# Kernel optimization log

Hardware: AMD Instinct MI355X
Metric: run time of the kernel (lower is better)

Reference implementation:

```python
import jax, jax.numpy as jnp
import numpy as np

EOS = 1e-10
N = 6000          # nnodes
E = 192000        # n_edges (avg degree 32)
D_IN = 512        # input_dim
H = 128           # hidden_dim
ALPHA = 1.0
TEMP = 1.0
BIAS = 1e-4


def setup_inputs() -> dict:
    key = jax.random.key(0)
    k1, k2, k3, k4, k5, k6, k7 = jax.random.split(key, 7)
    features = jax.random.normal(k1, (N, D_IN), dtype=jnp.float32)
    edges = jax.random.randint(k2, (2, E), 0, N)
    # params: embedding Linear(D_IN->H) and edge MLP Linear(2H->1)
    w_emb = jax.random.normal(k3, (D_IN, H), dtype=jnp.float32) * 0.05
    b_emb = jnp.zeros((H,), jnp.float32)
    w_mlp = jax.random.normal(k4, (2 * H, 1), dtype=jnp.float32) * 0.05
    b_mlp = jnp.zeros((1,), jnp.float32)
    # gumbel-sigmoid noise: eps = (bias-(1-bias))*u + (1-bias)  in [bias, 1-bias]
    u = jax.random.uniform(k5, (E,), dtype=jnp.float32)
    eps = (BIAS - (1.0 - BIAS)) * u + (1.0 - BIAS)
    gate_noise = jnp.log(eps) - jnp.log(1.0 - eps)
    return {"features": features, "edges": edges, "w_emb": w_emb, "b_emb": b_emb,
            "w_mlp": w_mlp, "b_mlp": b_mlp, "gate_noise": gate_noise}


def _normalize_sym(adj):
    d = adj.sum(axis=1)
    inv = 1.0 / (jnp.sqrt(d) + EOS)
    return adj * inv[:, None] * inv[None, :]


def reference(features, edges, w_emb, b_emb, w_mlp, b_mlp, gate_noise):
    # node embeddings: single Linear + ReLU
    emb = jax.nn.relu(features @ w_emb + b_emb)              # [N, H]
    h0 = emb[edges[0]]                                       # [E, H]
    h1 = emb[edges[1]]                                       # [E, H]
    s1 = (jnp.concatenate([h0, h1], axis=1) @ w_mlp + b_mlp).ravel()
    s2 = (jnp.concatenate([h1, h0], axis=1) @ w_mlp + b_mlp).ravel()
    raw = (s1 + s2) * 0.5                                    # [E]
    # gumbel-sigmoid gating
    weights_lp = jax.nn.sigmoid((gate_noise + raw) / TEMP)
    weights_hp = 1.0 - weights_lp

    eye = jnp.eye(N, dtype=features.dtype)

    def build_adj(w):
        adj = jnp.zeros((N, N), features.dtype).at[edges[0], edges[1]].set(w)
        return _normalize_sym(adj + eye)

    adj_lp = build_adj(weights_lp)
    adj_hp = build_adj(weights_hp)
    mask = jnp.zeros((N, N), features.dtype).at[edges[0], edges[1]].set(1.0)
    adj_hp = eye - adj_hp * mask * ALPHA
    adj_unnorm = jnp.zeros((N, N), features.dtype).at[edges[0], edges[1]].set(1.0)
    return (adj_lp, adj_hp, weights_lp, weights_hp, adj_unnorm)
```

## Files before the change

### kernel.cpp

```cpp
#include <hip/hip_runtime.h>
#include <math.h>

#define NNODES 6000
#define NEDGES 192000
#define DIN 512
#define HDIM 128
#define ALPHA 1.0f
#define EOS 1e-10f

static const size_t NN = (size_t)NNODES * (size_t)NNODES;

typedef float vfloat4 __attribute__((ext_vector_type(4)));

__global__ __launch_bounds__(256) void zero3_kernel(
    vfloat4* __restrict__ a, size_t na, vfloat4* __restrict__ b, size_t nb,
    vfloat4* __restrict__ c, size_t nc) {
  const size_t stride = (size_t)gridDim.x * blockDim.x;
  const size_t i = (size_t)blockIdx.x * blockDim.x + threadIdx.x;
  const vfloat4 z = {0.f, 0.f, 0.f, 0.f};
  for (size_t k = i; k < na; k += stride) __builtin_nontemporal_store(z, a + k);
  for (size_t k = i; k < nb; k += stride) __builtin_nontemporal_store(z, b + k);
  for (size_t k = i; k < nc; k += stride) c[k] = z;
}

__global__ __launch_bounds__(64) void embed_g_kernel(
    const float* __restrict__ feat, const float* __restrict__ w_emb,
    const float* __restrict__ b_emb, const float* __restrict__ w_mlp,
    const float* __restrict__ b_mlp, float* __restrict__ g) {
  __shared__ float sf[4 * DIN];
  const int t = threadIdx.x;
  const int nb = blockIdx.x * 4;

  const float4* f4 = (const float4*)(feat + (size_t)nb * DIN);
  float4* s4 = (float4*)sf;
#pragma unroll
  for (int k = 0; k < 8; ++k) s4[k * 64 + t] = f4[k * 64 + t];
  __syncthreads();

  const int h0 = t, h1 = t + 64;
  float acc0[4], acc1[4];
  const float b0 = b_emb[h0], b1 = b_emb[h1];
#pragma unroll
  for (int n = 0; n < 4; ++n) { acc0[n] = b0; acc1[n] = b1; }

  for (int d = 0; d < DIN; d += 4) {
    float w00 = w_emb[(d + 0) * HDIM + h0];
    float w01 = w_emb[(d + 1) * HDIM + h0];
    float w02 = w_emb[(d + 2) * HDIM + h0];
    float w03 = w_emb[(d + 3) * HDIM + h0];
    float w10 = w_emb[(d + 0) * HDIM + h1];
    float w11 = w_emb[(d + 1) * HDIM + h1];
    float w12 = w_emb[(d + 2) * HDIM + h1];
    float w13 = w_emb[(d + 3) * HDIM + h1];
#pragma unroll
    for (int n = 0; n < 4; ++n) {
      const float4 f = *(const float4*)&sf[n * DIN + d];
      acc0[n] += f.x * w00;
      acc0[n] += f.y * w01;
      acc0[n] += f.z * w02;
      acc0[n] += f.w * w03;
      acc1[n] += f.x * w10;
      acc1[n] += f.y * w11;
      acc1[n] += f.z * w12;
      acc1[n] += f.w * w13;
    }
  }

  const float wv0 = 0.5f * (w_mlp[h0] + w_mlp[HDIM + h0]);
  const float wv1 = 0.5f * (w_mlp[h1] + w_mlp[HDIM + h1]);
  const float half_b = 0.5f * b_mlp[0];
#pragma unroll
  for (int n = 0; n < 4; ++n) {
    float v = fmaxf(acc0[n], 0.0f) * wv0 + fmaxf(acc1[n], 0.0f) * wv1;
#pragma unroll
    for (int off = 32; off > 0; off >>= 1) v += __shfl_down(v, off, 64);
    if (t == 0) g[nb + n] = v + half_b;
  }
}

__global__ __launch_bounds__(256) void edge_weights_kernel(
    const int* __restrict__ edges, const float* __restrict__ g,
    const float* __restrict__ noise, float* __restrict__ w_lp,
    float* __restrict__ w_hp, int* __restrict__ winner) {
  const int e = blockIdx.x * blockDim.x + threadIdx.x;
  if (e >= NEDGES) return;
  const int u = edges[e];
  const int v = edges[NEDGES + e];
  const float x = noise[e] + g[u] + g[v];
  const float wl = 1.0f / (1.0f + expf(-x));
  const float wh = 1.0f - wl;
  w_lp[e] = wl;
  w_hp[e] = wh;
  atomicMax(&winner[(size_t)u * NNODES + v], e + 1);
}

__global__ __launch_bounds__(256) void edge_deg_kernel(
    const int* __restrict__ edges, const float* __restrict__ w_lp,
    const float* __restrict__ w_hp, const int* __restrict__ winner,
    float* __restrict__ deg_lp, float* __restrict__ deg_hp) {
  const int e = blockIdx.x * blockDim.x + threadIdx.x;
  if (e >= NEDGES) return;
  const int u = edges[e];
  const int v = edges[NEDGES + e];
  if (winner[(size_t)u * NNODES + v] != e + 1) return;
  atomicAdd(&deg_lp[u], w_lp[e]);
  atomicAdd(&deg_hp[u], w_hp[e]);
}

__global__ __launch_bounds__(256) void node_inv_kernel(
    const float* __restrict__ deg_lp, const float* __restrict__ deg_hp,
    float* __restrict__ inv_lp, float* __restrict__ inv_hp,
    float* __restrict__ adj_lp, float* __restrict__ adj_hp) {
  const int i = blockIdx.x * blockDim.x + threadIdx.x;
  if (i >= NNODES) return;
  const float il = 1.0f / (sqrtf(deg_lp[i] + 1.0f) + EOS);
  const float ih = 1.0f / (sqrtf(deg_hp[i] + 1.0f) + EOS);
  inv_lp[i] = il;
  inv_hp[i] = ih;
  const size_t diag = (size_t)i * NNODES + i;
  adj_lp[diag] = il * il;
  adj_hp[diag] = 1.0f;
}

__global__ __launch_bounds__(256) void edge_write_kernel(
    const int* __restrict__ edges, const float* __restrict__ w_lp,
    const float* __restrict__ w_hp, const float* __restrict__ inv_lp,
    const float* __restrict__ inv_hp, float* __restrict__ adj_lp,
    float* __restrict__ adj_hp, float* __restrict__ unnorm) {
  const int e = blockIdx.x * blockDim.x + threadIdx.x;
  if (e >= NEDGES) return;
  const int u = edges[e];
  const int v = edges[NEDGES + e];
  const size_t cell = (size_t)u * NNODES + v;
  const int win = ((const int*)unnorm)[cell];
  if (win != e + 1) return;
  const float wl = w_lp[e];
  const float wh = w_hp[e];
  const float il = inv_lp[u] * inv_lp[v];
  const float ih = inv_hp[u] * inv_hp[v];
  if (u == v) {
    adj_lp[cell] = (wl + 1.0f) * il;
    adj_hp[cell] = 1.0f - (wh + 1.0f) * ih * ALPHA;
  } else {
    adj_lp[cell] = wl * il;
    adj_hp[cell] = -wh * ih * ALPHA;
  }
  unnorm[cell] = 1.0f;
}

extern "C" void kernel_launch(void* const* d_in, const int* in_sizes, int n_in,
                              void* d_out, int out_size, void* d_ws,
                              size_t ws_size, hipStream_t stream) {
  const float* feat  = (const float*)d_in[0];
  const int*   edges = (const int*)d_in[1];
  const float* w_emb = (const float*)d_in[2];
  const float* b_emb = (const float*)d_in[3];
  const float* w_mlp = (const float*)d_in[4];
  const float* b_mlp = (const float*)d_in[5];
  const float* noise = (const float*)d_in[6];

  float* out    = (float*)d_out;
  float* adj_lp = out;
  float* adj_hp = out + NN;
  float* w_lp   = out + 2 * NN;
  float* w_hp   = w_lp + NEDGES;
  float* unnorm = w_hp + NEDGES;

  float* deg_lp = (float*)d_ws;
  float* deg_hp = deg_lp + NNODES;
  float* inv_lp = deg_hp + NNODES;
  float* inv_hp = inv_lp + NNODES;
  float* g      = inv_hp + NNODES;

  zero3_kernel<<<4096, 256, 0, stream>>>(
      (vfloat4*)adj_lp, (2 * NN) / 4, (vfloat4*)unnorm, NN / 4,
      (vfloat4*)deg_lp, (2 * NNODES) / 4);

  embed_g_kernel<<<NNODES / 4, 64, 0, stream>>>(feat, w_emb, b_emb, w_mlp,
                                                b_mlp, g);

  const int eb = (NEDGES + 255) / 256;
  edge_weights_kernel<<<eb, 256, 0, stream>>>(edges, g, noise, w_lp, w_hp,
                                              (int*)unnorm);
  edge_deg_kernel<<<eb, 256, 0, stream>>>(edges, w_lp, w_hp,
                                          (const int*)unnorm, deg_lp, deg_hp);
  node_inv_kernel<<<(NNODES + 255) / 256, 256, 0, stream>>>(
      deg_lp, deg_hp, inv_lp, inv_hp, adj_lp, adj_hp);
  edge_write_kernel<<<eb, 256, 0, stream>>>(edges, w_lp, w_hp, inv_lp, inv_hp,
                                            adj_lp, adj_hp, unnorm);
}
```

Before: 618.8 us.

## Fuse all stages into one cooperative kernel with grid-wide syncs

Replaces the six separate launches (zero, embed, edge weights, degree, inverse-sqrt, edge write) with a single cooperative kernel that uses grid.sync between phases. The embedding loop now processes 16 nodes per 256-thread block via a grid-stride loop. The aim is to remove per-launch overhead and inter-kernel gaps. In exchange it costs grid-wide barriers and a capped grid size that may lower memory-fill parallelism.

```diff
diff --git a/kernel.cpp b/kernel.cpp
--- a/kernel.cpp
+++ b/kernel.cpp
@@ -1,151 +1,154 @@
 #include <hip/hip_runtime.h>
+#include <hip/hip_cooperative_groups.h>
 #include <math.h>
+
+namespace cg = cooperative_groups;
 
 #define NNODES 6000
 #define NEDGES 192000
 #define DIN 512
 #define HDIM 128
-#define ALPHA 1.0f
 #define EOS 1e-10f
 
 static const size_t NN = (size_t)NNODES * (size_t)NNODES;
 
 typedef float vfloat4 __attribute__((ext_vector_type(4)));
 
-__global__ __launch_bounds__(256) void zero3_kernel(
-    vfloat4* __restrict__ a, size_t na, vfloat4* __restrict__ b, size_t nb,
-    vfloat4* __restrict__ c, size_t nc) {
-  const size_t stride = (size_t)gridDim.x * blockDim.x;
-  const size_t i = (size_t)blockIdx.x * blockDim.x + threadIdx.x;
-  const vfloat4 z = {0.f, 0.f, 0.f, 0.f};
-  for (size_t k = i; k < na; k += stride) __builtin_nontemporal_store(z, a + k);
-  for (size_t k = i; k < nb; k += stride) __builtin_nontemporal_store(z, b + k);
-  for (size_t k = i; k < nc; k += stride) c[k] = z;
-}
+__global__ __launch_bounds__(256, 3) void fused_kernel(
+    const float* __restrict__ feat, const int* __restrict__ edges,
+    const float* __restrict__ w_emb, const float* __restrict__ b_emb,
+    const float* __restrict__ w_mlp, const float* __restrict__ b_mlp,
+    const float* __restrict__ noise, float* __restrict__ adj_lp,
+    float* __restrict__ adj_hp, float* __restrict__ w_lp,
+    float* __restrict__ w_hp, float* __restrict__ unnorm,
+    float* __restrict__ deg_lp, float* __restrict__ deg_hp,
+    float* __restrict__ inv_lp, float* __restrict__ inv_hp,
+    float* __restrict__ g) {
+  cg::grid_group grid = cg::this_grid();
+  const int tid = threadIdx.x;
+  const size_t gtid = (size_t)blockIdx.x * blockDim.x + tid;
+  const size_t gstride = (size_t)gridDim.x * blockDim.x;
 
-__global__ __launch_bounds__(64) void embed_g_kernel(
-    const float* __restrict__ feat, const float* __restrict__ w_emb,
-    const float* __restrict__ b_emb, const float* __restrict__ w_mlp,
-    const float* __restrict__ b_mlp, float* __restrict__ g) {
-  __shared__ float sf[4 * DIN];
-  const int t = threadIdx.x;
-  const int nb = blockIdx.x * 4;
+  __shared__ float sf[16 * DIN];
 
-  const float4* f4 = (const float4*)(feat + (size_t)nb * DIN);
-  float4* s4 = (float4*)sf;
+  {
+    const vfloat4 z = {0.f, 0.f, 0.f, 0.f};
+    vfloat4* a = (vfloat4*)adj_lp;
+    for (size_t k = gtid; k < (2 * NN) / 4; k += gstride)
+      __builtin_nontemporal_store(z, a + k);
+    vfloat4* b = (vfloat4*)unnorm;
+    for (size_t k = gtid; k < NN / 4; k += gstride)
+      __builtin_nontemporal_store(z, b + k);
+    vfloat4* c = (vfloat4*)deg_lp;
+    for (size_t k = gtid; k < (2 * NNODES) / 4; k += gstride) c[k] = z;
+  }
+
+  for (int bg = blockIdx.x; bg < NNODES / 16; bg += gridDim.x) {
+    const float4* f4 = (const float4*)(feat + (size_t)bg * 16 * DIN);
+    float4* s4 = (float4*)sf;
 #pragma unroll
-  for (int k = 0; k < 8; ++k) s4[k * 64 + t] = f4[k * 64 + t];
-  __syncthreads();
+    for (int k = 0; k < 8; ++k) s4[k * 256 + tid] = f4[k * 256 + tid];
+    __syncthreads();
 
-  const int h0 = t, h1 = t + 64;
-  float acc0[4], acc1[4];
-  const float b0 = b_emb[h0], b1 = b_emb[h1];
+    const int wave = tid >> 6, lane = tid & 63;
+    const float* sw = sf + wave * (4 * DIN);
+    const int h0 = lane, h1 = lane + 64;
+    float acc0[4], acc1[4];
+    const float bb0 = b_emb[h0], bb1 = b_emb[h1];
 #pragma unroll
-  for (int n = 0; n < 4; ++n) { acc0[n] = b0; acc1[n] = b1; }
+    for (int n = 0; n < 4; ++n) { acc0[n] = bb0; acc1[n] = bb1; }
 
-  for (int d = 0; d < DIN; d += 4) {
-    float w00 = w_emb[(d + 0) * HDIM + h0];
-    float w01 = w_emb[(d + 1) * HDIM + h0];
-    float w02 = w_emb[(d + 2) * HDIM + h0];
-    float w03 = w_emb[(d + 3) * HDIM + h0];
-    float w10 = w_emb[(d + 0) * HDIM + h1];
-    float w11 = w_emb[(d + 1) * HDIM + h1];
-    float w12 = w_emb[(d + 2) * HDIM + h1];
-    float w13 = w_emb[(d + 3) * HDIM + h1];
+    for (int d = 0; d < DIN; d += 4) {
+      const float w00 = w_emb[(d + 0) * HDIM + h0];
+      const float w01 = w_emb[(d + 1) * HDIM + h0];
+      const float w02 = w_emb[(d + 2) * HDIM + h0];
+      const float w03 = w_emb[(d + 3) * HDIM + h0];
+      const float w10 = w_emb[(d + 0) * HDIM + h1];
+      const float w11 = w_emb[(d + 1) * HDIM + h1];
+      const float w12 = w_emb[(d + 2) * HDIM + h1];
+      const float w13 = w_emb[(d + 3) * HDIM + h1];
+#pragma unroll
+      for (int n = 0; n < 4; ++n) {
+        const float4 f = *(const float4*)&sw[n * DIN + d];
+        acc0[n] += f.x * w00;
+        acc0[n] += f.y * w01;
+        acc0[n] += f.z * w02;
+        acc0[n] += f.w * w03;
+        acc1[n] += f.x * w10;
+        acc1[n] += f.y * w11;
+        acc1[n] += f.z * w12;
+        acc1[n] += f.w * w13;
+      }
+    }
+
+    const float wv0 = 0.5f * (w_mlp[h0] + w_mlp[HDIM + h0]);
+    const float wv1 = 0.5f * (w_mlp[h1] + w_mlp[HDIM + h1]);
+    const float half_b = 0.5f * b_mlp[0];
+    const int node0 = bg * 16 + wave * 4;
 #pragma unroll
     for (int n = 0; n < 4; ++n) {
-      const float4 f = *(const float4*)&sf[n * DIN + d];
-      acc0[n] += f.x * w00;
-      acc0[n] += f.y * w01;
-      acc0[n] += f.z * w02;
-      acc0[n] += f.w * w03;
-      acc1[n] += f.x * w10;
-      acc1[n] += f.y * w11;
-      acc1[n] += f.z * w12;
-      acc1[n] += f.w * w13;
+      float v = fmaxf(acc0[n], 0.0f) * wv0 + fmaxf(acc1[n], 0.0f) * wv1;
+#pragma unroll
+      for (int off = 32; off > 0; off >>= 1) v += __shfl_down(v, off, 64);
+      if (lane == 0) g[node0 + n] = v + half_b;
     }
+    __syncthreads();
   }
 
-  const float wv0 = 0.5f * (w_mlp[h0] + w_mlp[HDIM + h0]);
-  const float wv1 = 0.5f * (w_mlp[h1] + w_mlp[HDIM + h1]);
-  const float half_b = 0.5f * b_mlp[0];
-#pragma unroll
-  for (int n = 0; n < 4; ++n) {
-    float v = fmaxf(acc0[n], 0.0f) * wv0 + fmaxf(acc1[n], 0.0f) * wv1;
-#pragma unroll
-    for (int off = 32; off > 0; off >>= 1) v += __shfl_down(v, off, 64);
-    if (t == 0) g[nb + n] = v + half_b;
+  grid.sync();
+
+  for (size_t e = gtid; e < NEDGES; e += gstride) {
+    const int u = edges[e];
+    const int v = edges[NEDGES + e];
+    const float x = noise[e] + g[u] + g[v];
+    const float wl = 1.0f / (1.0f + expf(-x));
+    w_lp[e] = wl;
+    w_hp[e] = 1.0f - wl;
+    atomicMax((int*)unnorm + ((size_t)u * NNODES + v), (int)e + 1);
   }
-}
 
-__global__ __launch_bounds__(256) void edge_weights_kernel(
-    const int* __restrict__ edges, const float* __restrict__ g,
-    const float* __restrict__ noise, float* __restrict__ w_lp,
-    float* __restrict__ w_hp, int* __restrict__ winner) {
-  const int e = blockIdx.x * blockDim.x + threadIdx.x;
-  if (e >= NEDGES) return;
-  const int u = edges[e];
-  const int v = edges[NEDGES + e];
-  const float x = noise[e] + g[u] + g[v];
-  const float wl = 1.0f / (1.0f + expf(-x));
-  const float wh = 1.0f - wl;
-  w_lp[e] = wl;
-  w_hp[e] = wh;
-  atomicMax(&winner[(size_t)u * NNODES + v], e + 1);
-}
+  grid.sync();
 
-__global__ __launch_bounds__(256) void edge_deg_kernel(
-    const int* __restrict__ edges, const float* __restrict__ w_lp,
-    const float* __restrict__ w_hp, const int* __restrict__ winner,
-    float* __restrict__ deg_lp, float* __restrict__ deg_hp) {
-  const int e = blockIdx.x * blockDim.x + threadIdx.x;
-  if (e >= NEDGES) return;
-  const int u = edges[e];
-  const int v = edges[NEDGES + e];
-  if (winner[(size_t)u * NNODES + v] != e + 1) return;
-  atomicAdd(&deg_lp[u], w_lp[e]);
-  atomicAdd(&deg_hp[u], w_hp[e]);
-}
+  for (size_t e = gtid; e < NEDGES; e += gstride) {
+    const int u = edges[e];
+    const int v = edges[NEDGES + e];
+    if (((const int*)unnorm)[(size_t)u * NNODES + v] != (int)e + 1) continue;
+    atomicAdd(&deg_lp[u], w_lp[e]);
+    atomicAdd(&deg_hp[u], w_hp[e]);
+  }
 
-__global__ __launch_bounds__(256) void node_inv_kernel(
-    const float* __restrict__ deg_lp, const float* __restrict__ deg_hp,
-    float* __restrict__ inv_lp, float* __restrict__ inv_hp,
-    float* __restrict__ adj_lp, float* __restrict__ adj_hp) {
-  const int i = blockIdx.x * blockDim.x + threadIdx.x;
-  if (i >= NNODES) return;
-  const float il = 1.0f / (sqrtf(deg_lp[i] + 1.0f) + EOS);
-  const float ih = 1.0f / (sqrtf(deg_hp[i] + 1.0f) + EOS);
-  inv_lp[i] = il;
-  inv_hp[i] = ih;
-  const size_t diag = (size_t)i * NNODES + i;
-  adj_lp[diag] = il * il;
-  adj_hp[diag] = 1.0f;
-}
+  grid.sync();
 
-__global__ __launch_bounds__(256) void edge_write_kernel(
-    const int* __restrict__ edges, const float* __restrict__ w_lp,
-    const float* __restrict__ w_hp, const float* __restrict__ inv_lp,
-    const float* __restrict__ inv_hp, float* __restrict__ adj_lp,
-    float* __restrict__ adj_hp, float* __restrict__ unnorm) {
-  const int e = blockIdx.x * blockDim.x + threadIdx.x;
-  if (e >= NEDGES) return;
-  const int u = edges[e];
-  const int v = edges[NEDGES + e];
-  const size_t cell = (size_t)u * NNODES + v;
-  const int win = ((const int*)unnorm)[cell];
-  if (win != e + 1) return;
-  const float wl = w_lp[e];
-  const float wh = w_hp[e];
-  const float il = inv_lp[u] * inv_lp[v];
-  const float ih = inv_hp[u] * inv_hp[v];
-  if (u == v) {
-    adj_lp[cell] = (wl + 1.0f) * il;
-    adj_hp[cell] = 1.0f - (wh + 1.0f) * ih * ALPHA;
-  } else {
-    adj_lp[cell] = wl * il;
-    adj_hp[cell] = -wh * ih * ALPHA;
+  for (size_t i = gtid; i < NNODES; i += gstride) {
+    const float il = 1.0f / (sqrtf(deg_lp[i] + 1.0f) + EOS);
+    const float ih = 1.0f / (sqrtf(deg_hp[i] + 1.0f) + EOS);
+    inv_lp[i] = il;
+    inv_hp[i] = ih;
+    const size_t dg = (size_t)i * NNODES + i;
+    adj_lp[dg] = il * il;
+    adj_hp[dg] = 1.0f;
   }
-  unnorm[cell] = 1.0f;
+
+  grid.sync();
+
+  for (size_t e = gtid; e < NEDGES; e += gstride) {
+    const int u = edges[e];
+    const int v = edges[NEDGES + e];
+    const size_t cell = (size_t)u * NNODES + v;
+    if (((const int*)unnorm)[cell] != (int)e + 1) continue;
+    const float wl = w_lp[e];
+    const float wh = w_hp[e];
+    const float il = inv_lp[u] * inv_lp[v];
+    const float ih = inv_hp[u] * inv_hp[v];
+    if (u == v) {
+      adj_lp[cell] = (wl + 1.0f) * il;
+      adj_hp[cell] = 1.0f - (wh + 1.0f) * ih;
+    } else {
+      adj_lp[cell] = wl * il;
+      adj_hp[cell] = -wh * ih;
+    }
+    unnorm[cell] = 1.0f;
+  }
 }
 
 extern "C" void kernel_launch(void* const* d_in, const int* in_sizes, int n_in,
@@ -172,20 +175,17 @@
   float* inv_hp = inv_lp + NNODES;
   float* g      = inv_hp + NNODES;
 
-  zero3_kernel<<<4096, 256, 0, stream>>>(
-      (vfloat4*)adj_lp, (2 * NN) / 4, (vfloat4*)unnorm, NN / 4,
-      (vfloat4*)deg_lp, (2 * NNODES) / 4);
+  int bpc = 0;
+  hipOccupancyMaxActiveBlocksPerMultiprocessor(&bpc, fused_kernel, 256, 0);
+  int nblk = bpc * 256;
+  if (nblk > 768) nblk = 768;
 
-  embed_g_kernel<<<NNODES / 4, 64, 0, stream>>>(feat, w_emb, b_emb, w_mlp,
-                                                b_mlp, g);
-
-  const int eb = (NEDGES + 255) / 256;
-  edge_weights_kernel<<<eb, 256, 0, stream>>>(edges, g, noise, w_lp, w_hp,
-                                              (int*)unnorm);
-  edge_deg_kernel<<<eb, 256, 0, stream>>>(edges, w_lp, w_hp,
-                                          (const int*)unnorm, deg_lp, deg_hp);
-  node_inv_kernel<<<(NNODES + 255) / 256, 256, 0, stream>>>(
-      deg_lp, deg_hp, inv_lp, inv_hp, adj_lp, adj_hp);
-  edge_write_kernel<<<eb, 256, 0, stream>>>(edges, w_lp, w_hp, inv_lp, inv_hp,
-                                            adj_lp, adj_hp, unnorm);
+  void* kargs[] = {(void*)&feat,   (void*)&edges,  (void*)&w_emb,
+                   (void*)&b_emb,  (void*)&w_mlp,  (void*)&b_mlp,
+                   (void*)&noise,  (void*)&adj_lp, (void*)&adj_hp,
+                   (void*)&w_lp,   (void*)&w_hp,   (void*)&unnorm,
+                   (void*)&deg_lp, (void*)&deg_hp, (void*)&inv_lp,
+                   (void*)&inv_hp, (void*)&g};
+  hipLaunchCooperativeKernel(fused_kernel, dim3(nblk), dim3(256), kargs, 0,
+                             stream);
 }
```

After: 812.9 us. 1.31x slower.

## Track duplicate-edge winners in a hash table instead of the dense matrix

Applied to the files above, without the earlier changes.

Edge deduplication now uses an open-addressing hash table in workspace (CAS on keys, atomicMax on values) rather than atomics on the dense unnorm matrix. This keeps scattered atomics and lookups in a small, cache-friendly region instead of a huge output buffer. The embedding kernel processes 8 nodes per block, and the zero kernel uses plain stores with a larger grid. It adds linear probing cost and zeroing of the table, and drops nontemporal stores.

```diff
diff --git a/kernel.cpp b/kernel.cpp
--- a/kernel.cpp
+++ b/kernel.cpp
@@ -5,21 +5,26 @@
 #define NEDGES 192000
 #define DIN 512
 #define HDIM 128
-#define ALPHA 1.0f
 #define EOS 1e-10f
 
+#define HSLOTS (1 << 20)
+#define HMASK (HSLOTS - 1)
+
 static const size_t NN = (size_t)NNODES * (size_t)NNODES;
 
-typedef float vfloat4 __attribute__((ext_vector_type(4)));
-
-__global__ __launch_bounds__(256) void zero3_kernel(
-    vfloat4* __restrict__ a, size_t na, vfloat4* __restrict__ b, size_t nb,
-    vfloat4* __restrict__ c, size_t nc) {
+__device__ __forceinline__ unsigned hash_cell(unsigned cell) {
+  return (cell * 2654435761u >> 11) & HMASK;
+}
+
+__global__ __launch_bounds__(256) void zero_kernel(
+    float4* __restrict__ a, size_t na,
+    float4* __restrict__ b, size_t nb,
+    float4* __restrict__ c, size_t nc) {
   const size_t stride = (size_t)gridDim.x * blockDim.x;
   const size_t i = (size_t)blockIdx.x * blockDim.x + threadIdx.x;
-  const vfloat4 z = {0.f, 0.f, 0.f, 0.f};
-  for (size_t k = i; k < na; k += stride) __builtin_nontemporal_store(z, a + k);
-  for (size_t k = i; k < nb; k += stride) __builtin_nontemporal_store(z, b + k);
+  const float4 z = make_float4(0.f, 0.f, 0.f, 0.f);
+  for (size_t k = i; k < na; k += stride) a[k] = z;
+  for (size_t k = i; k < nb; k += stride) b[k] = z;
   for (size_t k = i; k < nc; k += stride) c[k] = z;
 }
 
@@ -27,33 +32,33 @@
     const float* __restrict__ feat, const float* __restrict__ w_emb,
     const float* __restrict__ b_emb, const float* __restrict__ w_mlp,
     const float* __restrict__ b_mlp, float* __restrict__ g) {
-  __shared__ float sf[4 * DIN];
+  __shared__ float sf[8 * DIN];
   const int t = threadIdx.x;
-  const int nb = blockIdx.x * 4;
+  const int nb = blockIdx.x * 8;
 
   const float4* f4 = (const float4*)(feat + (size_t)nb * DIN);
   float4* s4 = (float4*)sf;
 #pragma unroll
-  for (int k = 0; k < 8; ++k) s4[k * 64 + t] = f4[k * 64 + t];
+  for (int k = 0; k < 16; ++k) s4[k * 64 + t] = f4[k * 64 + t];
   __syncthreads();
 
   const int h0 = t, h1 = t + 64;
-  float acc0[4], acc1[4];
+  float acc0[8], acc1[8];
   const float b0 = b_emb[h0], b1 = b_emb[h1];
 #pragma unroll
-  for (int n = 0; n < 4; ++n) { acc0[n] = b0; acc1[n] = b1; }
+  for (int n = 0; n < 8; ++n) { acc0[n] = b0; acc1[n] = b1; }
 
   for (int d = 0; d < DIN; d += 4) {
-    float w00 = w_emb[(d + 0) * HDIM + h0];
-    float w01 = w_emb[(d + 1) * HDIM + h0];
-    float w02 = w_emb[(d + 2) * HDIM + h0];
-    float w03 = w_emb[(d + 3) * HDIM + h0];
-    float w10 = w_emb[(d + 0) * HDIM + h1];
-    float w11 = w_emb[(d + 1) * HDIM + h1];
-    float w12 = w_emb[(d + 2) * HDIM + h1];
-    float w13 = w_emb[(d + 3) * HDIM + h1];
-#pragma unroll
-    for (int n = 0; n < 4; ++n) {
+    const float w00 = w_emb[(d + 0) * HDIM + h0];
+    const float w01 = w_emb[(d + 1) * HDIM + h0];
+    const float w02 = w_emb[(d + 2) * HDIM + h0];
+    const float w03 = w_emb[(d + 3) * HDIM + h0];
+    const float w10 = w_emb[(d + 0) * HDIM + h1];
+    const float w11 = w_emb[(d + 1) * HDIM + h1];
+    const float w12 = w_emb[(d + 2) * HDIM + h1];
+    const float w13 = w_emb[(d + 3) * HDIM + h1];
+#pragma unroll
+    for (int n = 0; n < 8; ++n) {
       const float4 f = *(const float4*)&sf[n * DIN + d];
       acc0[n] += f.x * w00;
       acc0[n] += f.y * w01;
@@ -70,7 +75,7 @@
   const float wv1 = 0.5f * (w_mlp[h1] + w_mlp[HDIM + h1]);
   const float half_b = 0.5f * b_mlp[0];
 #pragma unroll
-  for (int n = 0; n < 4; ++n) {
+  for (int n = 0; n < 8; ++n) {
     float v = fmaxf(acc0[n], 0.0f) * wv0 + fmaxf(acc1[n], 0.0f) * wv1;
 #pragma unroll
     for (int off = 32; off > 0; off >>= 1) v += __shfl_down(v, off, 64);
@@ -81,28 +86,45 @@
 __global__ __launch_bounds__(256) void edge_weights_kernel(
     const int* __restrict__ edges, const float* __restrict__ g,
     const float* __restrict__ noise, float* __restrict__ w_lp,
-    float* __restrict__ w_hp, int* __restrict__ winner) {
+    float* __restrict__ w_hp, int* __restrict__ hkeys,
+    int* __restrict__ hvals) {
   const int e = blockIdx.x * blockDim.x + threadIdx.x;
-  if (e >= NEDGES) return;
   const int u = edges[e];
   const int v = edges[NEDGES + e];
   const float x = noise[e] + g[u] + g[v];
   const float wl = 1.0f / (1.0f + expf(-x));
-  const float wh = 1.0f - wl;
   w_lp[e] = wl;
-  w_hp[e] = wh;
-  atomicMax(&winner[(size_t)u * NNODES + v], e + 1);
+  w_hp[e] = 1.0f - wl;
+
+  const unsigned cell = (unsigned)u * NNODES + (unsigned)v;
+  unsigned idx = hash_cell(cell);
+  const int key = (int)cell + 1;
+  while (true) {
+    const int k = atomicCAS(&hkeys[idx], 0, key);
+    if (k == 0 || k == key) { atomicMax(&hvals[idx], e + 1); break; }
+    idx = (idx + 1) & HMASK;
+  }
+}
+
+__device__ __forceinline__ int hash_winner(const int* __restrict__ hkeys,
+                                           const int* __restrict__ hvals,
+                                           unsigned cell) {
+  unsigned idx = hash_cell(cell);
+  const int key = (int)cell + 1;
+  while (hkeys[idx] != key) idx = (idx + 1) & HMASK;
+  return hvals[idx];
 }
 
 __global__ __launch_bounds__(256) void edge_deg_kernel(
     const int* __restrict__ edges, const float* __restrict__ w_lp,
-    const float* __restrict__ w_hp, const int* __restrict__ winner,
-    float* __restrict__ deg_lp, float* __restrict__ deg_hp) {
+    const float* __restrict__ w_hp, const int* __restrict__ hkeys,
+    const int* __restrict__ hvals, float* __restrict__ deg_lp,
+    float* __restrict__ deg_hp) {
   const int e = blockIdx.x * blockDim.x + threadIdx.x;
-  if (e >= NEDGES) return;
   const int u = edges[e];
   const int v = edges[NEDGES + e];
-  if (winner[(size_t)u * NNODES + v] != e + 1) return;
+  if (hash_winner(hkeys, hvals, (unsigned)u * NNODES + (unsigned)v) != e + 1)
+    return;
   atomicAdd(&deg_lp[u], w_lp[e]);
   atomicAdd(&deg_hp[u], w_hp[e]);
 }
@@ -117,33 +139,33 @@
   const float ih = 1.0f / (sqrtf(deg_hp[i] + 1.0f) + EOS);
   inv_lp[i] = il;
   inv_hp[i] = ih;
-  const size_t diag = (size_t)i * NNODES + i;
-  adj_lp[diag] = il * il;
-  adj_hp[diag] = 1.0f;
+  const size_t dg = (size_t)i * NNODES + i;
+  adj_lp[dg] = il * il;
+  adj_hp[dg] = 1.0f;
 }
 
 __global__ __launch_bounds__(256) void edge_write_kernel(
     const int* __restrict__ edges, const float* __restrict__ w_lp,
     const float* __restrict__ w_hp, const float* __restrict__ inv_lp,
-    const float* __restrict__ inv_hp, float* __restrict__ adj_lp,
+    const float* __restrict__ inv_hp, const int* __restrict__ hkeys,
+    const int* __restrict__ hvals, float* __restrict__ adj_lp,
     float* __restrict__ adj_hp, float* __restrict__ unnorm) {
   const int e = blockIdx.x * blockDim.x + threadIdx.x;
-  if (e >= NEDGES) return;
   const int u = edges[e];
   const int v = edges[NEDGES + e];
+  const unsigned cell32 = (unsigned)u * NNODES + (unsigned)v;
+  if (hash_winner(hkeys, hvals, cell32) != e + 1) return;
   const size_t cell = (size_t)u * NNODES + v;
-  const int win = ((const int*)unnorm)[cell];
-  if (win != e + 1) return;
   const float wl = w_lp[e];
   const float wh = w_hp[e];
   const float il = inv_lp[u] * inv_lp[v];
   const float ih = inv_hp[u] * inv_hp[v];
   if (u == v) {
     adj_lp[cell] = (wl + 1.0f) * il;
-    adj_hp[cell] = 1.0f - (wh + 1.0f) * ih * ALPHA;
+    adj_hp[cell] = 1.0f - (wh + 1.0f) * ih;
   } else {
     adj_lp[cell] = wl * il;
-    adj_hp[cell] = -wh * ih * ALPHA;
+    adj_hp[cell] = -wh * ih;
   }
   unnorm[cell] = 1.0f;
 }
@@ -166,26 +188,30 @@
   float* w_hp   = w_lp + NEDGES;
   float* unnorm = w_hp + NEDGES;
 
-  float* deg_lp = (float*)d_ws;
+  int*   hkeys  = (int*)d_ws;
+  int*   hvals  = hkeys + HSLOTS;
+  float* deg_lp = (float*)(hvals + HSLOTS);
   float* deg_hp = deg_lp + NNODES;
   float* inv_lp = deg_hp + NNODES;
   float* inv_hp = inv_lp + NNODES;
   float* g      = inv_hp + NNODES;
 
-  zero3_kernel<<<4096, 256, 0, stream>>>(
-      (vfloat4*)adj_lp, (2 * NN) / 4, (vfloat4*)unnorm, NN / 4,
-      (vfloat4*)deg_lp, (2 * NNODES) / 4);
-
-  embed_g_kernel<<<NNODES / 4, 64, 0, stream>>>(feat, w_emb, b_emb, w_mlp,
+  const size_t nc = (2 * (size_t)HSLOTS + 2 * NNODES) / 4;
+  zero_kernel<<<8192, 256, 0, stream>>>((float4*)adj_lp, (2 * NN) / 4,
+                                        (float4*)unnorm, NN / 4,
+                                        (float4*)hkeys, nc);
+
+  embed_g_kernel<<<NNODES / 8, 64, 0, stream>>>(feat, w_emb, b_emb, w_mlp,
                                                 b_mlp, g);
 
-  const int eb = (NEDGES + 255) / 256;
+  const int eb = NEDGES / 256;
   edge_weights_kernel<<<eb, 256, 0, stream>>>(edges, g, noise, w_lp, w_hp,
-                                              (int*)unnorm);
-  edge_deg_kernel<<<eb, 256, 0, stream>>>(edges, w_lp, w_hp,
-                                          (const int*)unnorm, deg_lp, deg_hp);
+                                              hkeys, hvals);
+  edge_deg_kernel<<<eb, 256, 0, stream>>>(edges, w_lp, w_hp, hkeys, hvals,
+                                          deg_lp, deg_hp);
   node_inv_kernel<<<(NNODES + 255) / 256, 256, 0, stream>>>(
       deg_lp, deg_hp, inv_lp, inv_hp, adj_lp, adj_hp);
   edge_write_kernel<<<eb, 256, 0, stream>>>(edges, w_lp, w_hp, inv_lp, inv_hp,
-                                            adj_lp, adj_hp, unnorm);
-}
+                                            hkeys, hvals, adj_lp, adj_hp,
+                                            unnorm);
+}
```

Result: no change. 609.8 us (-1.5%).
